# Performance work log

Hardware: AMD Instinct MI355X
Metric: run time of the kernel (lower is better)

Reference implementation:

```python
import jax, jax.numpy as jnp
import numpy as np

ENC_DIM = 1024
NUM_HEADS = 16
HEAD_DIM = ENC_DIM // NUM_HEADS
D_FF = 4 * ENC_DIM
EPS = 1e-5


def _layernorm(x, g, b):
    mu = jnp.mean(x, axis=-1, keepdims=True)
    var = jnp.mean((x - mu) ** 2, axis=-1, keepdims=True)
    return (x - mu) * jax.lax.rsqrt(var + EPS) * g + b


def setup_inputs() -> dict:
    key = jax.random.key(0)
    ks = jax.random.split(key, 12)
    s = 1.0 / np.sqrt(ENC_DIM)
    sf = 1.0 / np.sqrt(D_FF)
    x = jax.random.normal(ks[0], (2, 2048, ENC_DIM), dtype=jnp.float32)
    return {
        "x": x,
        "ln1_g": jnp.ones((ENC_DIM,), jnp.float32),
        "ln1_b": jnp.zeros((ENC_DIM,), jnp.float32),
        "wq": jax.random.uniform(ks[1], (ENC_DIM, ENC_DIM), jnp.float32, -s, s),
        "bq": jax.random.uniform(ks[2], (ENC_DIM,), jnp.float32, -s, s),
        "wk": jax.random.uniform(ks[3], (ENC_DIM, ENC_DIM), jnp.float32, -s, s),
        "bk": jax.random.uniform(ks[4], (ENC_DIM,), jnp.float32, -s, s),
        "wv": jax.random.uniform(ks[5], (ENC_DIM, ENC_DIM), jnp.float32, -s, s),
        "bv": jax.random.uniform(ks[6], (ENC_DIM,), jnp.float32, -s, s),
        "wo": jax.random.uniform(ks[7], (ENC_DIM, ENC_DIM), jnp.float32, -s, s),
        "bo": jax.random.uniform(ks[8], (ENC_DIM,), jnp.float32, -s, s),
        "w1": jax.random.uniform(ks[9], (ENC_DIM, D_FF), jnp.float32, -s, s),
        "b1": jax.random.uniform(ks[10], (D_FF,), jnp.float32, -s, s),
        "w2": jax.random.uniform(ks[11], (D_FF, ENC_DIM), jnp.float32, -sf, sf),
        "b2": jnp.zeros((ENC_DIM,), jnp.float32),
        "ln2_g": jnp.ones((ENC_DIM,), jnp.float32),
        "ln2_b": jnp.zeros((ENC_DIM,), jnp.float32),
    }


def reference(x, ln1_g, ln1_b, wq, bq, wk, bk, wv, bv, wo, bo, w1, b1, w2, b2, ln2_g, ln2_b):
    B, S, D = x.shape
    h = _layernorm(x, ln1_g, ln1_b)
    # QKV projections -> (B, H, S, hd)
    def split_heads(t):
        return t.reshape(B, S, NUM_HEADS, HEAD_DIM).transpose(0, 2, 1, 3)
    q = split_heads(h @ wq + bq)
    k = split_heads(h @ wk + bk)
    v = split_heads(h @ wv + bv)
    scores = jnp.einsum("bhqd,bhkd->bhqk", q, k) / np.sqrt(HEAD_DIM)
    probs = jax.nn.softmax(scores, axis=-1)
    attn = jnp.einsum("bhqk,bhkd->bhqd", probs, v)
    attn = attn.transpose(0, 2, 1, 3).reshape(B, S, D)
    x = attn @ wo + bo + x  # residual 1
    h2 = _layernorm(x, ln2_g, ln2_b)
    mlp = jax.nn.gelu(h2 @ w1 + b1, approximate=False) @ w2 + b2
    return x + mlp
```

## Files before the change

kernel.cpp:

```cpp
#include <hip/hip_runtime.h>

typedef unsigned short u16;
typedef unsigned int u32;
typedef __bf16 bf16x8 __attribute__((ext_vector_type(8)));
typedef float floatx4 __attribute__((ext_vector_type(4)));

__device__ __forceinline__ u16 f2bf(float f) {
    u32 u = __float_as_uint(f);
    u = (u + 0x7FFFu + ((u >> 16) & 1u)) >> 16;
    return (u16)u;
}

__device__ __forceinline__ void gld_lds16(const u16* g, u16* l) {
    __builtin_amdgcn_global_load_lds(
        (const __attribute__((address_space(1))) u32*)g,
        (__attribute__((address_space(3))) u32*)l, 16, 0, 0);
}

__device__ __forceinline__ float gelu_exact(float v) {
    const float z = fabsf(v) * 0.70710678118f;
    const float t = __builtin_amdgcn_rcpf(1.0f + 0.3275911f * z);
    const float e = __builtin_amdgcn_exp2f(-z * z * 1.44269504f);
    float poly = 1.061405429f;
    poly = poly * t - 1.453152027f;
    poly = poly * t + 1.421413741f;
    poly = poly * t - 0.284496736f;
    poly = poly * t + 0.254829592f;
    float erfz = 1.0f - poly * t * e;
    erfz = copysignf(erfz, v);
    return 0.5f * v * (1.0f + erfz);
}

__global__ __launch_bounds__(256) void transpose_cvt4(
    const float* __restrict__ s0, const float* __restrict__ s1,
    const float* __restrict__ s2, const float* __restrict__ s3,
    u16* __restrict__ d0, u16* __restrict__ d1,
    u16* __restrict__ d2, u16* __restrict__ d3)
{
    __shared__ float t[32][33];
    const int z = blockIdx.z;
    const float* src = z == 0 ? s0 : (z == 1 ? s1 : (z == 2 ? s2 : s3));
    u16* dst = z == 0 ? d0 : (z == 1 ? d1 : (z == 2 ? d2 : d3));
    const int bm = blockIdx.x * 32, bk = blockIdx.y * 32;
    const int tx = threadIdx.x & 31, ty = threadIdx.x >> 5;
    #pragma unroll
    for (int i = ty; i < 32; i += 8)
        t[i][tx] = src[(long)(bk + i) * 1024 + bm + tx];
    __syncthreads();
    #pragma unroll
    for (int i = ty; i < 32; i += 8)
        dst[(long)(bm + i) * 1024 + bk + tx] = f2bf(t[tx][i]);
}

__global__ __launch_bounds__(256) void transpose_cvt(
    const float* __restrict__ src, u16* __restrict__ dst, int K, int M)
{
    __shared__ float t[32][33];
    const int bm = blockIdx.x * 32, bk = blockIdx.y * 32;
    const int tx = threadIdx.x & 31, ty = threadIdx.x >> 5;
    #pragma unroll
    for (int i = ty; i < 32; i += 8)
        t[i][tx] = src[(long)(bk + i) * M + bm + tx];
    __syncthreads();
    #pragma unroll
    for (int i = ty; i < 32; i += 8)
        dst[(long)(bm + i) * K + bk + tx] = f2bf(t[tx][i]);
}

__global__ __launch_bounds__(256) void ln_kernel(
    const float* __restrict__ x, const float* __restrict__ g,
    const float* __restrict__ bta, u16* __restrict__ out)
{
    const int row = blockIdx.x;
    const int tid = threadIdx.x;
    const float4 v = ((const float4*)(x + (long)row * 1024))[tid];
    float s  = v.x + v.y + v.z + v.w;
    float s2 = v.x*v.x + v.y*v.y + v.z*v.z + v.w*v.w;
    #pragma unroll
    for (int off = 1; off < 64; off <<= 1) {
        s  += __shfl_xor(s, off);
        s2 += __shfl_xor(s2, off);
    }
    __shared__ float red[8];
    const int wave = tid >> 6, lane = tid & 63;
    if (lane == 0) { red[wave] = s; red[4 + wave] = s2; }
    __syncthreads();
    s  = red[0] + red[1] + red[2] + red[3];
    s2 = red[4] + red[5] + red[6] + red[7];
    const float mu   = s * (1.0f / 1024.0f);
    const float var  = s2 * (1.0f / 1024.0f) - mu * mu;
    const float rstd = rsqrtf(var + 1e-5f);
    const int c = tid << 2;
    ushort4 o;
    o.x = f2bf((v.x - mu) * rstd * g[c + 0] + bta[c + 0]);
    o.y = f2bf((v.y - mu) * rstd * g[c + 1] + bta[c + 1]);
    o.z = f2bf((v.z - mu) * rstd * g[c + 2] + bta[c + 2]);
    o.w = f2bf((v.w - mu) * rstd * g[c + 3] + bta[c + 3]);
    ((ushort4*)(out + (long)row * 1024))[tid] = o;
}

__global__ __launch_bounds__(256) void add_kernel(
    float* __restrict__ out, const float* __restrict__ p1)
{
    const int t = blockIdx.x * 256 + threadIdx.x;
    const float4 a = ((const float4*)out)[t];
    const float4 c = ((const float4*)p1)[t];
    float4 o;
    o.x = a.x + c.x;
    o.y = a.y + c.y;
    o.z = a.z + c.z;
    o.w = a.w + c.w;
    ((float4*)out)[t] = o;
}

__global__ __launch_bounds__(256) void vtrans_kernel(
    const u16* __restrict__ V, u16* __restrict__ Vt)
{
    __shared__ u16 t[64][72];
    const int bh = blockIdx.y, s0 = blockIdx.x << 6;
    const int tid = threadIdx.x;
    const long base = (long)bh * 2048 * 64;
    const int row = tid >> 2, seg = tid & 3;
    *(uint4*)&t[row][seg << 3] =
        *(const uint4*)(V + base + (long)(s0 + row) * 64 + (seg << 3));
    *(uint4*)&t[row][(seg + 4) << 3] =
        *(const uint4*)(V + base + (long)(s0 + row) * 64 + ((seg + 4) << 3));
    __syncthreads();
    #pragma unroll
    for (int half = 0; half < 2; ++half) {
        const int sl = (seg + (half << 2)) << 3;
        u16 tmp[8];
        #pragma unroll
        for (int j = 0; j < 8; ++j) tmp[j] = t[sl + j][row];
        *(uint4*)(Vt + base + (long)row * 2048 + s0 + sl) = *(uint4*)tmp;
    }
}

template<int MODE, int BN>
__global__ __launch_bounds__(256) void gemm_kernel(
    const u16* __restrict__ A, const u16* __restrict__ Bt,
    const float* __restrict__ bias0, const float* __restrict__ bias1,
    const float* __restrict__ bias2, const float* __restrict__ res,
    float* __restrict__ part1, void* __restrict__ outv, int K, int M)
{
    constexpr int MS  = (BN == 128) ? 4 : 2;
    constexpr int NIB = (BN == 128) ? 4 : 2;
    __shared__ u16 As[128 * 64];
    __shared__ u16 Bs[BN * 64];
    const int tid = threadIdx.x, lane = tid & 63, wave = tid >> 6;
    const int wm = (BN == 128) ? ((wave >> 1) << 6) : (wave << 5);
    const int wn = (BN == 128) ? ((wave & 1) << 6) : 0;
    const int lrow = lane & 15, quad = lane >> 4;
    const int sl = lrow & 7;

    const int nwg = gridDim.x * gridDim.y * gridDim.z;
    const int lin = blockIdx.x + gridDim.x * (blockIdx.y + gridDim.y * blockIdx.z);
    const int wg  = (lin & 7) * (nwg >> 3) + (lin >> 3);
    const int bx  = wg % gridDim.x;
    const int rest = wg / gridDim.x;
    const int by  = rest % gridDim.y;
    const int bz  = rest / gridDim.y;

    const long rowbase = (long)by * 128;
    const long colbase = (long)bx * BN;
    int kstart = 0, kend = K;
    if constexpr (MODE == 3) {
        kstart = bz * (K >> 1);
        kend   = kstart + (K >> 1);
    }

    const u16* gA[4]; int lA[4];
    #pragma unroll
    for (int i = 0; i < 4; ++i) {
        const int cid = (i << 6) + lane;
        const int rl = cid >> 3, p = cid & 7, q = p ^ (rl & 7);
        gA[i] = A + (rowbase + (wave << 5) + rl) * (long)K + kstart + (q << 3);
        lA[i] = ((wave << 5) + rl) * 64 + (p << 3);
    }
    const u16* gB[NIB]; int lB[NIB];
    #pragma unroll
    for (int i = 0; i < NIB; ++i) {
        const int cid = (i << 6) + lane;
        const int rl = cid >> 3, p = cid & 7, q = p ^ (rl & 7);
        const int rw = (BN == 128) ? (wave << 5) : (wave << 4);
        gB[i] = Bt + (colbase + rw + rl) * (long)K + kstart + (q << 3);
        lB[i] = (rw + rl) * 64 + (p << 3);
    }

    floatx4 acc[MS][4];
    #pragma unroll
    for (int i = 0; i < MS; ++i)
        #pragma unroll
        for (int j = 0; j < 4; ++j)
            acc[i][j] = floatx4{0.f, 0.f, 0.f, 0.f};

    for (int k0 = kstart; k0 < kend; k0 += 64) {
        __syncthreads();
        #pragma unroll
        for (int i = 0; i < 4; ++i) { gld_lds16(gA[i], As + lA[i]); gA[i] += 64; }
        #pragma unroll
        for (int i = 0; i < NIB; ++i) { gld_lds16(gB[i], Bs + lB[i]); gB[i] += 64; }
        __syncthreads();
        #pragma unroll
        for (int kc = 0; kc < 2; ++kc) {
            const int ph = (((kc << 2) + quad) ^ sl) << 3;
            bf16x8 af[MS], bf[4];
            #pragma unroll
            for (int ms = 0; ms < MS; ++ms)
                af[ms] = *(const bf16x8*)&As[(wm + (ms << 4) + lrow) * 64 + ph];
            #pragma unroll
            for (int ns = 0; ns < 4; ++ns)
                bf[ns] = *(const bf16x8*)&Bs[(wn + (ns << 4) + lrow) * 64 + ph];
            #pragma unroll
            for (int ms = 0; ms < MS; ++ms)
                #pragma unroll
                for (int ns = 0; ns < 4; ++ns)
                    acc[ms][ns] = __builtin_amdgcn_mfma_f32_16x16x32_bf16(
                        af[ms], bf[ns], acc[ms][ns], 0, 0, 0);
        }
    }

    float* tgt = nullptr;
    if constexpr (MODE == 3) tgt = bz ? part1 : (float*)outv;
    #pragma unroll
    for (int ms = 0; ms < MS; ++ms) {
        #pragma unroll
        for (int ns = 0; ns < 4; ++ns) {
            const long col = colbase + wn + (ns << 4) + lrow;
            float bv = 0.f;
            if constexpr (MODE == 0) {
                const int which = (int)(col >> 10);
                const float* bp = which == 0 ? bias0 : (which == 1 ? bias1 : bias2);
                bv = bp[col & 1023];
            } else if constexpr (MODE == 1 || MODE == 2) {
                bv = bias0[col];
            }
            #pragma unroll
            for (int r = 0; r < 4; ++r) {
                const long row = rowbase + wm + (ms << 4) + (quad << 2) + r;
                float v = acc[ms][ns][r] + bv;
                if constexpr (MODE == 0) {
                    const long which = col >> 10;
                    if (which == 0) v *= 0.18033688f;
                    const long b = row >> 11, s = row & 2047;
                    const long h = (col >> 6) & 15, d = col & 63;
                    ((u16*)outv)[which * 4194304 + (((b << 4) + h) * 2048 + s) * 64 + d] = f2bf(v);
                } else if constexpr (MODE == 1) {
                    const long idx = row * M + col;
                    ((float*)outv)[idx] = v + res[idx];
                } else if constexpr (MODE == 2) {
                    ((u16*)outv)[row * M + col] = f2bf(gelu_exact(v));
                } else {
                    const long idx = row * M + col;
                    if (bz == 0)
                        tgt[idx] = v + bias0[col] + res[idx];
                    else
                        tgt[idx] = v;
                }
            }
        }
    }
}

__global__ __launch_bounds__(512) void attn_kernel(
    const u16* __restrict__ Q, const u16* __restrict__ Kp,
    const u16* __restrict__ Vt, u16* __restrict__ O)
{
    __shared__ u16 Ks[2][4096];
    __shared__ u16 Vs[2][4096];
    __shared__ u16 Ps[8][16][72];
    const int tid = threadIdx.x, lane = tid & 63, wave = tid >> 6;
    const int lrow = lane & 15, quad = lane >> 4;

    const int lin = blockIdx.x;
    const int nl  = ((lin & 7) << 6) + (lin >> 3);
    const int bh  = nl >> 4;
    const int qt  = nl & 15;
    const long kvbase = (long)bh * 2048 * 64;
    const int qbase = (qt << 7) + (wave << 4);

    const int srow = lane >> 3;
    const int schunk = (lane & 7) ^ srow;
    const int c = wave & 3;
    const bool isV = wave >= 4;
    const int lofs = c << 10;
    const u16* g0 = isV
        ? (Vt + kvbase + (long)(((c << 4) + srow) * 2048 + (schunk << 3)))
        : (Kp + kvbase + (long)(((c << 4) + srow) * 64   + (schunk << 3)));
    const u16* g1 = g0 + (isV ? 8 * 2048 : 8 * 64);
    const int gstep = isV ? 64 : 4096;
    u16* lb0 = isV ? &Vs[0][lofs] : &Ks[0][lofs];
    u16* lb1 = isV ? &Vs[1][lofs] : &Ks[1][lofs];

    bf16x8 qf[2];
    #pragma unroll
    for (int h = 0; h < 2; ++h)
        qf[h] = *(const bf16x8*)(Q + kvbase +
            (long)(qbase + lrow) * 64 + (quad << 3) + (h << 5));

    int aoff[4][2];
    #pragma unroll
    for (int ns = 0; ns < 4; ++ns)
        #pragma unroll
        for (int h = 0; h < 2; ++h)
            aoff[ns][h] = ((ns << 4) + lrow) * 64 +
                          (((quad + (h << 2)) ^ (lrow & 7)) << 3);

    floatx4 oacc[4];
    #pragma unroll
    for (int ns = 0; ns < 4; ++ns)
        oacc[ns] = floatx4{0.f, 0.f, 0.f, 0.f};
    float lr = 0.f;

    gld_lds16(g0, lb0);
    gld_lds16(g1, lb0 + 512);
    g0 += gstep; g1 += gstep;

    for (int it = 0; it < 32; ++it) {
        const int cur = it & 1;
        __syncthreads();
        if (it < 31) {
            u16* dst = cur ? lb0 : lb1;
            gld_lds16(g0, dst);
            gld_lds16(g1, dst + 512);
            g0 += gstep; g1 += gstep;
        }
        const u16* ks = &Ks[cur][0];
        const u16* vs = &Vs[cur][0];

        floatx4 st[4];
        __builtin_amdgcn_s_setprio(1);
        #pragma unroll
        for (int ns = 0; ns < 4; ++ns) {
            const bf16x8 af0 = *(const bf16x8*)&ks[aoff[ns][0]];
            const bf16x8 af1 = *(const bf16x8*)&ks[aoff[ns][1]];
            floatx4 z = floatx4{0.f, 0.f, 0.f, 0.f};
            st[ns] = __builtin_amdgcn_mfma_f32_16x16x32_bf16(af0, qf[0], z, 0, 0, 0);
            st[ns] = __builtin_amdgcn_mfma_f32_16x16x32_bf16(af1, qf[1], st[ns], 0, 0, 0);
        }
        __builtin_amdgcn_s_setprio(0);

        float rs = 0.f;
        #pragma unroll
        for (int ns = 0; ns < 4; ++ns) {
            const float p0 = __builtin_amdgcn_exp2f(st[ns][0]);
            const float p1 = __builtin_amdgcn_exp2f(st[ns][1]);
            const float p2 = __builtin_amdgcn_exp2f(st[ns][2]);
            const float p3 = __builtin_amdgcn_exp2f(st[ns][3]);
            rs += (p0 + p1) + (p2 + p3);
            uint2 w;
            w.x = __builtin_amdgcn_perm(__float_as_uint(p1) + 0x8000u,
                                        __float_as_uint(p0) + 0x8000u, 0x07060302u);
            w.y = __builtin_amdgcn_perm(__float_as_uint(p3) + 0x8000u,
                                        __float_as_uint(p2) + 0x8000u, 0x07060302u);
            *(uint2*)&Ps[wave][lrow][(ns << 4) + (quad << 2)] = w;
        }
        rs += __shfl_xor(rs, 16);
        rs += __shfl_xor(rs, 32);
        lr += rs;
        const bf16x8 pf0 = *(const bf16x8*)&Ps[wave][lrow][quad << 3];
        const bf16x8 pf1 = *(const bf16x8*)&Ps[wave][lrow][(quad << 3) + 32];

        __builtin_amdgcn_s_setprio(1);
        #pragma unroll
        for (int ns = 0; ns < 4; ++ns) {
            const bf16x8 vf0 = *(const bf16x8*)&vs[aoff[ns][0]];
            const bf16x8 vf1 = *(const bf16x8*)&vs[aoff[ns][1]];
            oacc[ns] = __builtin_amdgcn_mfma_f32_16x16x32_bf16(pf0, vf0, oacc[ns], 0, 0, 0);
            oacc[ns] = __builtin_amdgcn_mfma_f32_16x16x32_bf16(pf1, vf1, oacc[ns], 0, 0, 0);
        }
        __builtin_amdgcn_s_setprio(0);
    }

    const int b = bh >> 4, h = bh & 15;
    float linv[4];
    #pragma unroll
    for (int r = 0; r < 4; ++r)
        linv[r] = 1.0f / __shfl(lr, (quad << 2) + r);
    #pragma unroll
    for (int ns = 0; ns < 4; ++ns)
        #pragma unroll
        for (int r = 0; r < 4; ++r) {
            const int q = qbase + (quad << 2) + r;
            const long token = (long)b * 2048 + q;
            O[token * 1024 + (h << 6) + (ns << 4) + lrow] =
                f2bf(oacc[ns][r] * linv[r]);
        }
}

extern "C" void kernel_launch(void* const* d_in, const int* in_sizes, int n_in,
                              void* d_out, int out_size, void* d_ws, size_t ws_size,
                              hipStream_t stream)
{
    const float* x     = (const float*)d_in[0];
    const float* ln1_g = (const float*)d_in[1];
    const float* ln1_b = (const float*)d_in[2];
    const float* wq    = (const float*)d_in[3];
    const float* bq    = (const float*)d_in[4];
    const float* wk    = (const float*)d_in[5];
    const float* bk    = (const float*)d_in[6];
    const float* wv    = (const float*)d_in[7];
    const float* bv    = (const float*)d_in[8];
    const float* wo    = (const float*)d_in[9];
    const float* bo    = (const float*)d_in[10];
    const float* w1    = (const float*)d_in[11];
    const float* b1    = (const float*)d_in[12];
    const float* w2    = (const float*)d_in[13];
    const float* b2    = (const float*)d_in[14];
    const float* ln2_g = (const float*)d_in[15];
    const float* ln2_b = (const float*)d_in[16];
    float* out = (float*)d_out;

    char* w = (char*)d_ws;
    const size_t MB = 1024 * 1024;
    u16*   wqkvt = (u16*)(w + 0);
    u16*   wot   = (u16*)(w + 6  * MB);
    u16*   w1t   = (u16*)(w + 8  * MB);
    u16*   w2t   = (u16*)(w + 16 * MB);
    u16*   h1    = (u16*)(w + 24 * MB);
    u16*   qkvb  = (u16*)(w + 32 * MB);
    u16*   vtb   = (u16*)(w + 56 * MB);
    float* x1    = (float*)(w + 64 * MB);
    float* part1 = (float*)(w + 80 * MB);
    u16*   ffb   = (u16*)(w + 32 * MB);
    u16*   qb = qkvb;
    u16*   kb = qkvb + 4194304;
    u16*   vb = qkvb + 8388608;

    transpose_cvt4<<<dim3(32, 32, 4), 256, 0, stream>>>(
        wq, wk, wv, wo, wqkvt, wqkvt + 1048576, wqkvt + 2097152, wot);
    transpose_cvt<<<dim3(128, 32), 256, 0, stream>>>(w1, w1t, 1024, 4096);
    transpose_cvt<<<dim3(32, 128), 256, 0, stream>>>(w2, w2t, 4096, 1024);

    ln_kernel<<<4096, 256, 0, stream>>>(x, ln1_g, ln1_b, h1);

    gemm_kernel<0, 128><<<dim3(24, 32), 256, 0, stream>>>(
        h1, wqkvt, bq, bk, bv, nullptr, nullptr, qkvb, 1024, 3072);

    vtrans_kernel<<<dim3(32, 32), 256, 0, stream>>>(vb, vtb);

    attn_kernel<<<dim3(512), 512, 0, stream>>>(qb, kb, vtb, h1);

    gemm_kernel<1, 64><<<dim3(16, 32), 256, 0, stream>>>(
        h1, wot, bo, nullptr, nullptr, x, nullptr, x1, 1024, 1024);

    ln_kernel<<<4096, 256, 0, stream>>>(x1, ln2_g, ln2_b, h1);

    gemm_kernel<2, 128><<<dim3(32, 32), 256, 0, stream>>>(
        h1, w1t, b1, nullptr, nullptr, nullptr, nullptr, ffb, 1024, 4096);

    gemm_kernel<3, 64><<<dim3(16, 32, 2), 256, 0, stream>>>(
        ffb, w2t, b2, nullptr, nullptr, x1, part1, out, 4096, 1024);

    add_kernel<<<4096, 256, 0, stream>>>(out, part1);
}
```

Baseline: 379.9 us.

## Double-buffer GEMM LDS tiles to overlap global loads with MFMA

Allocates two LDS buffers for the A and B tiles and issues the next k-tile's global-to-LDS loads before computing on the current tile. Partial vmcnt waits and raw barriers replace the two __syncthreads per iteration, so memory latency can hide behind MFMA work. This doubles LDS usage per block, which may reduce occupancy, and relies on hand-counted vmcnt values matching the number of outstanding loads.

```diff
diff --git a/kernel.cpp b/kernel.cpp
--- a/kernel.cpp
+++ b/kernel.cpp
@@ -145,8 +145,8 @@
 {
     constexpr int MS  = (BN == 128) ? 4 : 2;
     constexpr int NIB = (BN == 128) ? 4 : 2;
-    __shared__ u16 As[128 * 64];
-    __shared__ u16 Bs[BN * 64];
+    __shared__ u16 As[2][128 * 64];
+    __shared__ u16 Bs[2][BN * 64];
     const int tid = threadIdx.x, lane = tid & 63, wave = tid >> 6;
     const int wm = (BN == 128) ? ((wave >> 1) << 6) : (wave << 5);
     const int wn = (BN == 128) ? ((wave & 1) << 6) : 0;
@@ -194,23 +194,38 @@
         for (int j = 0; j < 4; ++j)
             acc[i][j] = floatx4{0.f, 0.f, 0.f, 0.f};
 
-    for (int k0 = kstart; k0 < kend; k0 += 64) {
-        __syncthreads();
-        #pragma unroll
-        for (int i = 0; i < 4; ++i) { gld_lds16(gA[i], As + lA[i]); gA[i] += 64; }
-        #pragma unroll
-        for (int i = 0; i < NIB; ++i) { gld_lds16(gB[i], Bs + lB[i]); gB[i] += 64; }
-        __syncthreads();
+    #pragma unroll
+    for (int i = 0; i < 4; ++i) { gld_lds16(gA[i], As[0] + lA[i]); gA[i] += 64; }
+    #pragma unroll
+    for (int i = 0; i < NIB; ++i) { gld_lds16(gB[i], Bs[0] + lB[i]); gB[i] += 64; }
+
+    const int niter = (kend - kstart) >> 6;
+    int cur = 0;
+    for (int t = 0; t < niter; ++t) {
+        if (t + 1 < niter) {
+            #pragma unroll
+            for (int i = 0; i < 4; ++i) { gld_lds16(gA[i], As[cur ^ 1] + lA[i]); gA[i] += 64; }
+            #pragma unroll
+            for (int i = 0; i < NIB; ++i) { gld_lds16(gB[i], Bs[cur ^ 1] + lB[i]); gB[i] += 64; }
+            if constexpr (BN == 128) asm volatile("s_waitcnt vmcnt(8)" ::: "memory");
+            else                     asm volatile("s_waitcnt vmcnt(6)" ::: "memory");
+        } else {
+            asm volatile("s_waitcnt vmcnt(0)" ::: "memory");
+        }
+        __builtin_amdgcn_s_barrier();
+
+        const u16* as = As[cur];
+        const u16* bs = Bs[cur];
         #pragma unroll
         for (int kc = 0; kc < 2; ++kc) {
             const int ph = (((kc << 2) + quad) ^ sl) << 3;
             bf16x8 af[MS], bf[4];
             #pragma unroll
             for (int ms = 0; ms < MS; ++ms)
-                af[ms] = *(const bf16x8*)&As[(wm + (ms << 4) + lrow) * 64 + ph];
+                af[ms] = *(const bf16x8*)&as[(wm + (ms << 4) + lrow) * 64 + ph];
             #pragma unroll
             for (int ns = 0; ns < 4; ++ns)
-                bf[ns] = *(const bf16x8*)&Bs[(wn + (ns << 4) + lrow) * 64 + ph];
+                bf[ns] = *(const bf16x8*)&bs[(wn + (ns << 4) + lrow) * 64 + ph];
             #pragma unroll
             for (int ms = 0; ms < MS; ++ms)
                 #pragma unroll
@@ -218,6 +233,9 @@
                     acc[ms][ns] = __builtin_amdgcn_mfma_f32_16x16x32_bf16(
                         af[ms], bf[ns], acc[ms][ns], 0, 0, 0);
         }
+        asm volatile("s_waitcnt lgkmcnt(0)" ::: "memory");
+        __builtin_amdgcn_s_barrier();
+        cur ^= 1;
     }
 
     float* tgt = nullptr;
```

After: 384.1 us. No clear change (+1.1%).
